# Kernel optimization log

Hardware: AMD Instinct MI355X
Metric: run time of the kernel (lower is better)

The kernel has to match this reference:

```python
import jax, jax.numpy as jnp
import numpy as np

NUM_HEADS = 8
ATTN_LEN = 5


def setup_inputs() -> dict:
    rng = jax.random.key(0)
    ks = jax.random.split(rng, 10)
    B, T, D = 2, 4096, 1024
    H, HD = NUM_HEADS, D // NUM_HEADS
    n = lambda k, shape, scale=1.0: jax.random.normal(k, shape, jnp.float32) * scale
    return {
        "query": n(ks[0], (B, T, D)),
        "key": n(ks[1], (B, T, D)),
        "value": n(ks[2], (B, T, D)),
        "Wq": n(ks[3], (D, D), 0.02),
        "bq": jnp.zeros((D,), jnp.float32),
        "Wk": n(ks[4], (D, D), 0.02),
        "bk": jnp.zeros((D,), jnp.float32),
        "Wv": n(ks[5], (D, D), 0.02),
        "bv": jnp.zeros((D,), jnp.float32),
        "Er": n(ks[6], (H, HD, ATTN_LEN)),
        "layer": 1,
    }


def _forward(query, key, value, Wq, bq, Wk, bk, Wv, bv, Er, layer):
    B, T, D = query.shape
    H = NUM_HEADS
    HD = D // H
    dil = 2 ** layer
    pad = dil * (ATTN_LEN // 2)
    Tp = T + 2 * pad

    # torch nn.Linear: y = x @ W^T + b ; reshape to [B, H, T, HD]
    q = (query @ Wq.T + bq).reshape(B, T, H, HD).transpose(0, 2, 1, 3)
    k = (key @ Wk.T + bk).reshape(B, T, H, HD).transpose(0, 2, 1, 3)
    v = (value @ Wv.T + bv).reshape(B, T, H, HD).transpose(0, 2, 1, 3)

    # head-group source mapping + shifts (note k head 7 reuses k head 6, per source)
    src_k = jnp.array([0, 1, 2, 3, 4, 5, 6, 6])
    src_v = jnp.array([0, 1, 2, 3, 4, 5, 6, 7])
    shifts = jnp.array([0, 0, 0, 0, -2, -1, 1, 2])

    # kv_roll equivalence: window slot j at time t for shift s reads
    # padded[(t + (s + j) * dil) mod Tp]  (torch.roll wraparound included)
    t_idx = jnp.arange(T)
    j_idx = jnp.arange(ATTN_LEN)
    idx = (t_idx[None, :, None] + (shifts[:, None, None] + j_idx[None, None, :]) * dil) % Tp  # [H,T,L]

    def windows(x, src):
        xp = jnp.pad(x, ((0, 0), (0, 0), (pad, pad), (0, 0)))[:, src]  # [B,H,Tp,HD]
        g = jnp.take_along_axis(xp, idx.reshape(1, H, T * ATTN_LEN, 1), axis=2)
        return g.reshape(B, H, T, ATTN_LEN, HD)

    kw = windows(k, src_k)  # [B,H,T,L,HD]
    vw = windows(v, src_v)

    qk = jnp.einsum('bhtd,bhtjd->bhtj', q, kw)            # [B,H,T,L]
    mask = jnp.where(qk == 0.0, -jnp.inf, 0.0)            # zero dot product => padding
    qer = jnp.einsum('bhtd,hdj->bhtj', q, Er)             # relative positional bias
    attn = jax.nn.softmax((qk + qer) / np.sqrt(HD).astype(np.float32) + mask, axis=-1)
    out = jnp.einsum('bhtj,bhtjd->bhtd', attn, vw)        # [B,H,T,HD]
    out = out.transpose(0, 2, 1, 3).reshape(B, T, D)
    return out, attn[:, :, :, None, :]                     # attn shaped [B,H,T,1,L] like torch


def reference(query, key, value, Wq, bq, Wk, bk, Wv, bv, Er, layer):
    return _forward(query, key, value, Wq, bq, Wk, bk, Wv, bv, Er, layer)
```

## Files before the change

### kernel.cpp

```cpp
#include <hip/hip_runtime.h>
#include <hip/hip_bf16.h>

constexpr int B_ = 2, T_ = 4096, D_ = 1024, H_ = 8, HD_ = 128, L_ = 5;
constexpr int M_ = B_ * T_;
constexpr int K_ = D_;
constexpr int N_ = D_;
constexpr int TB_ = 64;
constexpr int NSMAX_ = 96;

typedef __attribute__((ext_vector_type(8))) __bf16 bf16x8;
typedef __attribute__((ext_vector_type(4))) float f32x4;

__device__ __constant__ int c_srck[8]  = {0, 1, 2, 3, 4, 5, 6, 6};
__device__ __constant__ int c_shift[8] = {0, 0, 0, 0, -2, -1, 1, 2};

__device__ __forceinline__ void gload_lds16(const void* g, void* l) {
    __builtin_amdgcn_global_load_lds(
        (__attribute__((address_space(1))) void*)g,
        (__attribute__((address_space(3))) void*)l, 16, 0, 0);
}

__global__ __launch_bounds__(256) void cvt_kernel(
    const float* __restrict__ q,  const float* __restrict__ k,  const float* __restrict__ v,
    const float* __restrict__ wq, const float* __restrict__ wk, const float* __restrict__ wv,
    __hip_bfloat16* __restrict__ qb,  __hip_bfloat16* __restrict__ kb,  __hip_bfloat16* __restrict__ vb,
    __hip_bfloat16* __restrict__ wqb, __hip_bfloat16* __restrict__ wkb, __hip_bfloat16* __restrict__ wvb)
{
    const int y = blockIdx.y;
    const float* src;
    __hip_bfloat16* dst;
    size_t idx;
    if (blockIdx.x < 4096) {
        src = (y == 0) ? q : (y == 1) ? k : v;
        dst = (y == 0) ? qb : (y == 1) ? kb : vb;
        idx = ((size_t)blockIdx.x * 256 + threadIdx.x) * 8;
    } else {
        src = (y == 0) ? wq : (y == 1) ? wk : wv;
        dst = (y == 0) ? wqb : (y == 1) ? wkb : wvb;
        idx = ((size_t)(blockIdx.x - 4096) * 256 + threadIdx.x) * 8;
    }
    f32x4 a = *(const f32x4*)(const void*)(src + idx);
    f32x4 b = *(const f32x4*)(const void*)(src + idx + 4);
    bf16x8 o;
#pragma unroll
    for (int e = 0; e < 4; ++e) { o[e] = (__bf16)a[e]; o[e + 4] = (__bf16)b[e]; }
    *(bf16x8*)(void*)(dst + idx) = o;
}

__global__ __launch_bounds__(256) void qkv_gemm_bf16(
    const __hip_bfloat16* __restrict__ qb,
    const __hip_bfloat16* __restrict__ kb,
    const __hip_bfloat16* __restrict__ vb,
    const __hip_bfloat16* __restrict__ wqb,
    const __hip_bfloat16* __restrict__ wkb,
    const __hip_bfloat16* __restrict__ wvb,
    const float* __restrict__ bq,
    const float* __restrict__ bk,
    const float* __restrict__ bv,
    __hip_bfloat16* __restrict__ qout,
    __hip_bfloat16* __restrict__ kout,
    __hip_bfloat16* __restrict__ vout)
{
    const int z = blockIdx.z;
    const __hip_bfloat16* A = (z == 0) ? qb  : (z == 1) ? kb  : vb;
    const __hip_bfloat16* W = (z == 0) ? wqb : (z == 1) ? wkb : wvb;
    const float* bias       = (z == 0) ? bq  : (z == 1) ? bk  : bv;
    __hip_bfloat16* C       = (z == 0) ? qout : (z == 1) ? kout : vout;

    __shared__ __align__(16) __hip_bfloat16 As[128 * 32];
    __shared__ __align__(16) __hip_bfloat16 Bs[128 * 32];

    const int tid  = threadIdx.x;
    const int wave = tid >> 6;
    const int lane = tid & 63;
    const int m0 = blockIdx.x * 128;
    const int n0 = blockIdx.y * 128;
    const int wm = (wave >> 1) * 64;
    const int wn = (wave & 1) * 64;

    f32x4 acc[4][4];
#pragma unroll
    for (int i = 0; i < 4; ++i)
#pragma unroll
        for (int j = 0; j < 4; ++j)
            acc[i][j] = (f32x4){0.f, 0.f, 0.f, 0.f};

    const int srow = lane >> 2;
    const int scol = (lane & 3) * 8;

    const int fr = lane & 15;
    const int fk = (lane >> 4) * 8;

    for (int k0 = 0; k0 < K_; k0 += 32) {
#pragma unroll
        for (int r = 0; r < 2; ++r) {
            const int issue = wave + r * 4;
            const int row = issue * 16 + srow;
            gload_lds16(A + (size_t)(m0 + row) * K_ + k0 + scol,
                        (void*)(As + issue * 512));
            gload_lds16(W + (size_t)(n0 + row) * K_ + k0 + scol,
                        (void*)(Bs + issue * 512));
        }
        __syncthreads();

        bf16x8 af[4], bf[4];
#pragma unroll
        for (int i = 0; i < 4; ++i) {
            af[i] = *(const bf16x8*)(const void*)(As + (wm + i * 16 + fr) * 32 + fk);
            bf[i] = *(const bf16x8*)(const void*)(Bs + (wn + i * 16 + fr) * 32 + fk);
        }
#pragma unroll
        for (int i = 0; i < 4; ++i)
#pragma unroll
            for (int j = 0; j < 4; ++j)
                acc[i][j] = __builtin_amdgcn_mfma_f32_16x16x32_bf16(
                    af[i], bf[j], acc[i][j], 0, 0, 0);
        __syncthreads();
    }

    const int col_l = lane & 15;
    const int row_l = (lane >> 4) * 4;
#pragma unroll
    for (int j = 0; j < 4; ++j) {
        const int n = n0 + wn + j * 16 + col_l;
        const float bval = bias[n];
#pragma unroll
        for (int i = 0; i < 4; ++i) {
            const int m = m0 + wm + i * 16 + row_l;
#pragma unroll
            for (int r = 0; r < 4; ++r)
                C[(size_t)(m + r) * N_ + n] = __float2bfloat16(acc[i][j][r] + bval);
        }
    }
}

__global__ __launch_bounds__(256) void qkv_gemm_f32(
    const float* __restrict__ query,
    const float* __restrict__ key,
    const float* __restrict__ value,
    const float* __restrict__ Wq,
    const float* __restrict__ bq,
    const float* __restrict__ Wk,
    const float* __restrict__ bk,
    const float* __restrict__ Wv,
    const float* __restrict__ bv,
    __hip_bfloat16* __restrict__ qout,
    __hip_bfloat16* __restrict__ kout,
    __hip_bfloat16* __restrict__ vout)
{
    const int z = blockIdx.z;
    const float* A    = (z == 0) ? query : (z == 1) ? key : value;
    const float* W    = (z == 0) ? Wq    : (z == 1) ? Wk  : Wv;
    const float* bias = (z == 0) ? bq    : (z == 1) ? bk  : bv;
    __hip_bfloat16* C = (z == 0) ? qout  : (z == 1) ? kout : vout;

    __shared__ __align__(16) float As[128 * 32];
    __shared__ __align__(16) float Bs[128 * 32];

    const int tid  = threadIdx.x;
    const int wave = tid >> 6;
    const int lane = tid & 63;
    const int m0 = blockIdx.x * 128;
    const int n0 = blockIdx.y * 128;
    const int wm = (wave >> 1) * 64;
    const int wn = (wave & 1) * 64;

    f32x4 acc[4][4];
#pragma unroll
    for (int i = 0; i < 4; ++i)
#pragma unroll
        for (int j = 0; j < 4; ++j)
            acc[i][j] = (f32x4){0.f, 0.f, 0.f, 0.f};

    const int srow = lane >> 3;
    const int lcg  = (lane & 7) ^ srow;
    const int gcol = lcg * 4;

    const int fr  = lane & 15;
    const int r7  = fr & 7;
    const int cgA = (lane >> 4) * 2;
    const int pcg0 = (cgA)     ^ r7;
    const int pcg1 = (cgA ^ 1) ^ r7;

    for (int k0 = 0; k0 < K_; k0 += 32) {
#pragma unroll
        for (int r = 0; r < 4; ++r) {
            const int issue = wave + r * 4;
            const int row = issue * 8 + srow;
            gload_lds16(A + (size_t)(m0 + row) * K_ + k0 + gcol,
                        (void*)(As + issue * 256));
            gload_lds16(W + (size_t)(n0 + row) * K_ + k0 + gcol,
                        (void*)(Bs + issue * 256));
        }
        __syncthreads();

        bf16x8 af[4], bf[4];
#pragma unroll
        for (int i = 0; i < 4; ++i) {
            const float* ap = As + (wm + i * 16 + fr) * 32;
            f32x4 a0 = *(const f32x4*)(const void*)(ap + pcg0 * 4);
            f32x4 a1 = *(const f32x4*)(const void*)(ap + pcg1 * 4);
            const float* bp = Bs + (wn + i * 16 + fr) * 32;
            f32x4 b0 = *(const f32x4*)(const void*)(bp + pcg0 * 4);
            f32x4 b1 = *(const f32x4*)(const void*)(bp + pcg1 * 4);
#pragma unroll
            for (int e = 0; e < 4; ++e) {
                af[i][e]     = (__bf16)a0[e];
                af[i][e + 4] = (__bf16)a1[e];
                bf[i][e]     = (__bf16)b0[e];
                bf[i][e + 4] = (__bf16)b1[e];
            }
        }
#pragma unroll
        for (int i = 0; i < 4; ++i)
#pragma unroll
            for (int j = 0; j < 4; ++j)
                acc[i][j] = __builtin_amdgcn_mfma_f32_16x16x32_bf16(
                    af[i], bf[j], acc[i][j], 0, 0, 0);
        __syncthreads();
    }

    const int col_l = lane & 15;
    const int row_l = (lane >> 4) * 4;
#pragma unroll
    for (int j = 0; j < 4; ++j) {
        const int n = n0 + wn + j * 16 + col_l;
        const float bval = bias[n];
#pragma unroll
        for (int i = 0; i < 4; ++i) {
            const int m = m0 + wm + i * 16 + row_l;
#pragma unroll
            for (int r = 0; r < 4; ++r)
                C[(size_t)(m + r) * N_ + n] = __float2bfloat16(acc[i][j][r] + bval);
        }
    }
}

__global__ __launch_bounds__(256) void attn_kernel(
    const __hip_bfloat16* __restrict__ qp,
    const __hip_bfloat16* __restrict__ kp,
    const __hip_bfloat16* __restrict__ vp,
    const float* __restrict__ Er,
    const int* __restrict__ layer_p,
    float* __restrict__ out,
    float* __restrict__ attn_out)
{
    const int dil = 1 << (*layer_p);
    int NS = TB_ + 4 * dil;
    if (NS > NSMAX_) NS = NSMAX_;

    const int tid = threadIdx.x;
    const int t0 = blockIdx.x * TB_;
    const int h  = blockIdx.y;
    const int b  = blockIdx.z;
    const int shift = c_shift[h];
    const int srck  = c_srck[h];
    const int off_lo = (shift - 2) * dil;

    __shared__ __align__(16) __hip_bfloat16 Ks[NSMAX_ * 128];
    __shared__ __align__(16) __hip_bfloat16 Vs[NSMAX_ * 128];
    __shared__ __align__(16) float ErT[5][128];

    for (int i = tid; i < 640; i += 256) {
        const int d = i / 5, j = i - d * 5;
        ErT[j][d] = Er[(size_t)h * 640 + i];
    }

    const int sr = tid >> 4;
    const int sc = tid & 15;
    for (int i0 = 0; i0 < NS; i0 += 16) {
        const int i = i0 + sr;
        if (i < NS) {
            const int r = t0 + off_lo + i;
            bf16x8 kv8 = (bf16x8){0, 0, 0, 0, 0, 0, 0, 0};
            bf16x8 vv8 = (bf16x8){0, 0, 0, 0, 0, 0, 0, 0};
            if (r >= 0 && r < T_) {
                kv8 = *(const bf16x8*)(const void*)(
                    kp + (size_t)(b * T_ + r) * D_ + srck * HD_ + sc * 8);
                vv8 = *(const bf16x8*)(const void*)(
                    vp + (size_t)(b * T_ + r) * D_ + h * HD_ + sc * 8);
            }
            const int pc = sc ^ (i & 3);
            *(bf16x8*)(void*)(Ks + i * 128 + pc * 8) = kv8;
            *(bf16x8*)(void*)(Vs + i * 128 + pc * 8) = vv8;
        }
    }
    __syncthreads();

    const int lr = tid >> 2;
    const int ld = tid & 3;
    const int t  = t0 + lr;
    const size_t qoff = (size_t)(b * T_ + t) * D_ + h * HD_ + ld * 32;

    float qf[32];
#pragma unroll
    for (int c = 0; c < 4; ++c) {
        bf16x8 qv = *(const bf16x8*)(const void*)(qp + qoff + c * 8);
#pragma unroll
        for (int e = 0; e < 8; ++e) qf[c * 8 + e] = (float)qv[e];
    }

    float lg[5];
    bool  valid[5];
    int   irow[5];
#pragma unroll
    for (int j = 0; j < 5; ++j) {
        const int i = lr + j * dil;
        irow[j] = i;
        const int orig = t + (shift + j - 2) * dil;
        valid[j] = (orig >= 0) && (orig < T_);

        float s = 0.f;
#pragma unroll
        for (int c = 0; c < 4; ++c) {
            const int pc = (ld * 4 + c) ^ (i & 3);
            bf16x8 kk = *(const bf16x8*)(const void*)(Ks + i * 128 + pc * 8);
#pragma unroll
            for (int e = 0; e < 8; ++e) s += qf[c * 8 + e] * (float)kk[e];
        }
        if (!valid[j]) s = 0.f;
#pragma unroll
        for (int c = 0; c < 8; ++c) {
            f32x4 ev = *(const f32x4*)(const void*)(&ErT[j][ld * 32 + c * 4]);
#pragma unroll
            for (int e = 0; e < 4; ++e) s += qf[c * 4 + e] * ev[e];
        }
        s += __shfl_xor(s, 1, 4);
        s += __shfl_xor(s, 2, 4);
        lg[j] = valid[j] ? s * 0.08838834764831845f : -INFINITY;
    }

    float mx = lg[0];
#pragma unroll
    for (int j = 1; j < 5; ++j) mx = fmaxf(mx, lg[j]);
    float w[5], sum = 0.f;
#pragma unroll
    for (int j = 0; j < 5; ++j) {
        w[j] = valid[j] ? __expf(lg[j] - mx) : 0.f;
        sum += w[j];
    }
    const float inv = 1.f / sum;
#pragma unroll
    for (int j = 0; j < 5; ++j) w[j] *= inv;

    float o[32];
#pragma unroll
    for (int m = 0; m < 32; ++m) o[m] = 0.f;
#pragma unroll
    for (int j = 0; j < 5; ++j) {
        const int i = irow[j];
#pragma unroll
        for (int c = 0; c < 4; ++c) {
            const int pc = (ld * 4 + c) ^ (i & 3);
            bf16x8 vv = *(const bf16x8*)(const void*)(Vs + i * 128 + pc * 8);
#pragma unroll
            for (int e = 0; e < 8; ++e) o[c * 8 + e] += w[j] * (float)vv[e];
        }
    }

#pragma unroll
    for (int c = 0; c < 8; ++c) {
        f32x4 ov = (f32x4){o[c * 4], o[c * 4 + 1], o[c * 4 + 2], o[c * 4 + 3]};
        *(f32x4*)(void*)(out + qoff + c * 4) = ov;
    }

    const size_t abase = ((size_t)(b * H_ + h) * T_ + t) * L_;
    attn_out[abase + ld] = w[ld];
    if (ld == 0) attn_out[abase + 4] = w[4];
}

extern "C" void kernel_launch(void* const* d_in, const int* in_sizes, int n_in,
                              void* d_out, int out_size, void* d_ws, size_t ws_size,
                              hipStream_t stream) {
    const float* query = (const float*)d_in[0];
    const float* key   = (const float*)d_in[1];
    const float* value = (const float*)d_in[2];
    const float* Wq    = (const float*)d_in[3];
    const float* bq    = (const float*)d_in[4];
    const float* Wk    = (const float*)d_in[5];
    const float* bk    = (const float*)d_in[6];
    const float* Wv    = (const float*)d_in[7];
    const float* bv    = (const float*)d_in[8];
    const float* Er    = (const float*)d_in[9];
    const int*   layer = (const int*)d_in[10];

    float* out  = (float*)d_out;
    float* attn = out + (size_t)B_ * T_ * D_;

    const size_t SA = (size_t)M_ * K_;
    const size_t SW = (size_t)N_ * K_;
    const size_t SP = (size_t)M_ * N_;
    const size_t need = (3 * SA + 3 * SW + 3 * SP) * sizeof(__hip_bfloat16);

    char* ws = (char*)d_ws;
    if (ws_size >= need) {
        __hip_bfloat16* qb  = (__hip_bfloat16*)ws;
        __hip_bfloat16* kb  = qb + SA;
        __hip_bfloat16* vb  = kb + SA;
        __hip_bfloat16* wqb = vb + SA;
        __hip_bfloat16* wkb = wqb + SW;
        __hip_bfloat16* wvb = wkb + SW;
        __hip_bfloat16* qp  = wvb + SW;
        __hip_bfloat16* kp  = qp + SP;
        __hip_bfloat16* vp  = kp + SP;

        cvt_kernel<<<dim3(4608, 3), 256, 0, stream>>>(
            query, key, value, Wq, Wk, Wv, qb, kb, vb, wqb, wkb, wvb);

        qkv_gemm_bf16<<<dim3(M_ / 128, N_ / 128, 3), 256, 0, stream>>>(
            qb, kb, vb, wqb, wkb, wvb, bq, bk, bv, qp, kp, vp);

        attn_kernel<<<dim3(T_ / TB_, H_, B_), 256, 0, stream>>>(
            qp, kp, vp, Er, layer, out, attn);
    } else {
        __hip_bfloat16* qp = (__hip_bfloat16*)ws;
        __hip_bfloat16* kp = qp + SP;
        __hip_bfloat16* vp = kp + SP;

        qkv_gemm_f32<<<dim3(M_ / 128, N_ / 128, 3), 256, 0, stream>>>(
            query, key, value, Wq, bq, Wk, bk, Wv, bv, qp, kp, vp);

        attn_kernel<<<dim3(T_ / TB_, H_, B_), 256, 0, stream>>>(
            qp, kp, vp, Er, layer, out, attn);
    }
}
```

Baseline: 255.2 us.

## Replace QKV GEMM with 256x256 double-buffered ping-pong pipelined bf16 kernel

Rewrites the bf16 projection GEMM to use 256x256 tiles with BK=64, 512 threads and double-buffered LDS. Global-to-LDS loads for the next tile are interleaved with four MFMA quadrants, with explicit barriers, waitcnts and s_setprio controlling the schedule. LDS rows are XOR-swizzled to avoid bank conflicts. The aim is to raise arithmetic intensity and hide load latency behind compute. In exchange, register pressure is higher and the hand-scheduled synchronisation is fragile.

Result: slower. 260.5 us (+2.1%).

```diff
diff --git a/kernel.cpp b/kernel.cpp
--- a/kernel.cpp
+++ b/kernel.cpp
@@ -7,6 +7,10 @@
 constexpr int N_ = D_;
 constexpr int TB_ = 64;
 constexpr int NSMAX_ = 96;
+
+constexpr int BM_ = 256, BN_ = 256, BKG_ = 64;
+constexpr int NT_ = K_ / BKG_;
+constexpr int TILEG_ = BM_ * BKG_;
 
 typedef __attribute__((ext_vector_type(8))) __bf16 bf16x8;
 typedef __attribute__((ext_vector_type(4))) float f32x4;
@@ -47,7 +51,7 @@
     *(bf16x8*)(void*)(dst + idx) = o;
 }
 
-__global__ __launch_bounds__(256) void qkv_gemm_bf16(
+__global__ __launch_bounds__(512, 2) void qkv_gemm_8ph(
     const __hip_bfloat16* __restrict__ qb,
     const __hip_bfloat16* __restrict__ kb,
     const __hip_bfloat16* __restrict__ vb,
@@ -67,69 +71,140 @@
     const float* bias       = (z == 0) ? bq  : (z == 1) ? bk  : bv;
     __hip_bfloat16* C       = (z == 0) ? qout : (z == 1) ? kout : vout;
 
-    __shared__ __align__(16) __hip_bfloat16 As[128 * 32];
-    __shared__ __align__(16) __hip_bfloat16 Bs[128 * 32];
+    __shared__ __align__(16) __hip_bfloat16 As[2][TILEG_];
+    __shared__ __align__(16) __hip_bfloat16 Bs[2][TILEG_];
 
     const int tid  = threadIdx.x;
     const int wave = tid >> 6;
     const int lane = tid & 63;
-    const int m0 = blockIdx.x * 128;
-    const int n0 = blockIdx.y * 128;
-    const int wm = (wave >> 1) * 64;
-    const int wn = (wave & 1) * 64;
-
-    f32x4 acc[4][4];
-#pragma unroll
-    for (int i = 0; i < 4; ++i)
-#pragma unroll
-        for (int j = 0; j < 4; ++j)
-            acc[i][j] = (f32x4){0.f, 0.f, 0.f, 0.f};
-
-    const int srow = lane >> 2;
-    const int scol = (lane & 3) * 8;
+    const int m0 = blockIdx.x * BM_;
+    const int n0 = blockIdx.y * BN_;
+    const int wm = (wave >> 2) * 128;
+    const int wn = (wave & 3) * 64;
+
+    f32x4 acc[8][4];
+#pragma unroll
+    for (int i = 0; i < 8; ++i)
+#pragma unroll
+        for (int j = 0; j < 4; ++j) acc[i][j] = (f32x4){0.f, 0.f, 0.f, 0.f};
+
+    const int srow = tid >> 3;
+    const int sch  = (tid & 7) ^ (srow & 7);
+    const __hip_bfloat16* aSrc = A + (size_t)(m0 + srow) * K_ + sch * 8;
+    const __hip_bfloat16* bSrc = W + (size_t)(n0 + srow) * K_ + sch * 8;
+    const int wdst = wave * 512;
+
+    auto stageA = [&](int buf, int h, int t) {
+        const __hip_bfloat16* s = aSrc + (size_t)h * (128 * K_) + t * BKG_;
+        __hip_bfloat16* d = &As[buf][h * 8192 + wdst];
+        gload_lds16(s, d);
+        gload_lds16(s + (size_t)64 * K_, d + 4096);
+    };
+    auto stageB = [&](int buf, int h, int t) {
+        const __hip_bfloat16* s = bSrc + (size_t)h * (128 * K_) + t * BKG_;
+        __hip_bfloat16* d = &Bs[buf][h * 8192 + wdst];
+        gload_lds16(s, d);
+        gload_lds16(s + (size_t)64 * K_, d + 4096);
+    };
 
     const int fr = lane & 15;
-    const int fk = (lane >> 4) * 8;
-
-    for (int k0 = 0; k0 < K_; k0 += 32) {
-#pragma unroll
-        for (int r = 0; r < 2; ++r) {
-            const int issue = wave + r * 4;
-            const int row = issue * 16 + srow;
-            gload_lds16(A + (size_t)(m0 + row) * K_ + k0 + scol,
-                        (void*)(As + issue * 512));
-            gload_lds16(W + (size_t)(n0 + row) * K_ + k0 + scol,
-                        (void*)(Bs + issue * 512));
-        }
-        __syncthreads();
-
-        bf16x8 af[4], bf[4];
-#pragma unroll
-        for (int i = 0; i < 4; ++i) {
-            af[i] = *(const bf16x8*)(const void*)(As + (wm + i * 16 + fr) * 32 + fk);
-            bf[i] = *(const bf16x8*)(const void*)(Bs + (wn + i * 16 + fr) * 32 + fk);
-        }
-#pragma unroll
-        for (int i = 0; i < 4; ++i)
-#pragma unroll
-            for (int j = 0; j < 4; ++j)
-                acc[i][j] = __builtin_amdgcn_mfma_f32_16x16x32_bf16(
-                    af[i], bf[j], acc[i][j], 0, 0, 0);
-        __syncthreads();
+    const int fx = lane >> 4;
+    const int c0 = ((0 + fx) ^ (fr & 7)) * 8;
+    const int c1 = ((4 + fx) ^ (fr & 7)) * 8;
+
+    bf16x8 a[4][2], b0[2][2], b1[2][2];
+
+    auto lda = [&](int buf, int mh) {
+        const __hip_bfloat16* p = &As[buf][(wm + mh * 64 + fr) * 64];
+#pragma unroll
+        for (int mi = 0; mi < 4; ++mi) {
+            a[mi][0] = *(const bf16x8*)(const void*)(p + mi * 1024 + c0);
+            a[mi][1] = *(const bf16x8*)(const void*)(p + mi * 1024 + c1);
+        }
+    };
+    auto ldb = [&](bf16x8 (&bf)[2][2], int buf, int nh) {
+        const __hip_bfloat16* p = &Bs[buf][(wn + nh * 32 + fr) * 64];
+#pragma unroll
+        for (int nj = 0; nj < 2; ++nj) {
+            bf[nj][0] = *(const bf16x8*)(const void*)(p + nj * 1024 + c0);
+            bf[nj][1] = *(const bf16x8*)(const void*)(p + nj * 1024 + c1);
+        }
+    };
+    auto mfma_q = [&](int mh, int nh, bf16x8 (&bf)[2][2]) {
+#pragma unroll
+        for (int kk = 0; kk < 2; ++kk)
+#pragma unroll
+            for (int mi = 0; mi < 4; ++mi)
+#pragma unroll
+                for (int nj = 0; nj < 2; ++nj)
+                    acc[mh * 4 + mi][nh * 2 + nj] =
+                        __builtin_amdgcn_mfma_f32_16x16x32_bf16(
+                            a[mi][kk], bf[nj][kk],
+                            acc[mh * 4 + mi][nh * 2 + nj], 0, 0, 0);
+    };
+
+    stageA(0, 0, 0); stageB(0, 0, 0);
+    stageA(0, 1, 0); stageB(0, 1, 0);
+    stageB(1, 0, 1); stageA(1, 0, 1);
+    asm volatile("s_waitcnt vmcnt(4)" ::: "memory");
+    __builtin_amdgcn_s_barrier();
+
+#pragma unroll 1
+    for (int t = 0; t < NT_; ++t) {
+        const int buf = t & 1, nbuf = buf ^ 1;
+
+        lda(buf, 0); ldb(b0, buf, 0);
+        if (t + 1 < NT_) stageA(nbuf, 1, t + 1);
+        __builtin_amdgcn_s_barrier();
+        asm volatile("s_waitcnt lgkmcnt(0)" ::: "memory");
+        __builtin_amdgcn_sched_barrier(0);
+        __builtin_amdgcn_s_setprio(1);
+        mfma_q(0, 0, b0);
+        __builtin_amdgcn_s_setprio(0);
+        __builtin_amdgcn_s_barrier();
+
+        ldb(b1, buf, 1);
+        if (t + 1 < NT_) stageB(nbuf, 1, t + 1);
+        __builtin_amdgcn_s_barrier();
+        asm volatile("s_waitcnt lgkmcnt(0)" ::: "memory");
+        __builtin_amdgcn_sched_barrier(0);
+        __builtin_amdgcn_s_setprio(1);
+        mfma_q(0, 1, b1);
+        __builtin_amdgcn_s_setprio(0);
+        __builtin_amdgcn_s_barrier();
+
+        lda(buf, 1);
+        if (t + 2 < NT_) stageB(buf, 0, t + 2);
+        __builtin_amdgcn_s_barrier();
+        asm volatile("s_waitcnt lgkmcnt(0)" ::: "memory");
+        __builtin_amdgcn_sched_barrier(0);
+        __builtin_amdgcn_s_setprio(1);
+        mfma_q(1, 1, b1);
+        __builtin_amdgcn_s_setprio(0);
+        __builtin_amdgcn_s_barrier();
+
+        if (t + 2 < NT_) stageA(buf, 0, t + 2);
+        __builtin_amdgcn_s_barrier();
+        __builtin_amdgcn_s_setprio(1);
+        mfma_q(1, 0, b0);
+        __builtin_amdgcn_s_setprio(0);
+        if (t < NT_ - 2) asm volatile("s_waitcnt vmcnt(4)" ::: "memory");
+        else             asm volatile("s_waitcnt vmcnt(0)" ::: "memory");
+        __builtin_amdgcn_s_barrier();
     }
 
     const int col_l = lane & 15;
     const int row_l = (lane >> 4) * 4;
 #pragma unroll
-    for (int j = 0; j < 4; ++j) {
-        const int n = n0 + wn + j * 16 + col_l;
+    for (int J = 0; J < 4; ++J) {
+        const int n = n0 + wn + J * 16 + col_l;
         const float bval = bias[n];
 #pragma unroll
-        for (int i = 0; i < 4; ++i) {
-            const int m = m0 + wm + i * 16 + row_l;
+        for (int I = 0; I < 8; ++I) {
+            const int m = m0 + wm + I * 16 + row_l;
 #pragma unroll
             for (int r = 0; r < 4; ++r)
-                C[(size_t)(m + r) * N_ + n] = __float2bfloat16(acc[i][j][r] + bval);
+                C[(size_t)(m + r) * N_ + n] = __float2bfloat16(acc[I][J][r] + bval);
         }
     }
 }
@@ -407,7 +482,7 @@
         cvt_kernel<<<dim3(4608, 3), 256, 0, stream>>>(
             query, key, value, Wq, Wk, Wv, qb, kb, vb, wqb, wkb, wvb);
 
-        qkv_gemm_bf16<<<dim3(M_ / 128, N_ / 128, 3), 256, 0, stream>>>(
+        qkv_gemm_8ph<<<dim3(M_ / BM_, N_ / BN_, 3), 512, 0, stream>>>(
             qb, kb, vb, wqb, wkb, wvb, bq, bk, bv, qp, kp, vp);
 
         attn_kernel<<<dim3(T_ / TB_, H_, B_), 256, 0, stream>>>(
```
